# Kernel optimization log

Measured on AMD Instinct MI355X. Metric: run time of the kernel, lower is better.

Reference implementation:

```python
import jax, jax.numpy as jnp
import numpy as np

N_QUBITS = 8
EMBED_DIM = 1024
FFN_DIM = 4096


def _apply_1q_batched(state, gate, wire):
    # state: [N] + [2]*n ; gate: [N,2,2] (per-sample)
    n = state.ndim - 1
    N = state.shape[0]
    L = 2 ** wire
    R = 2 ** (n - 1 - wire)
    st = state.reshape(N, L, 2, R)
    st = jnp.einsum('nba,nlar->nlbr', gate, st)
    return st.reshape((N,) + (2,) * n)


def _apply_1q_shared(state, gate, wire):
    # gate: [2,2] shared across samples
    n = state.ndim - 1
    N = state.shape[0]
    L = 2 ** wire
    R = 2 ** (n - 1 - wire)
    st = state.reshape(N, L, 2, R)
    st = jnp.einsum('ba,nlar->nlbr', gate, st)
    return st.reshape((N,) + (2,) * n)


def _cnot(state, control, target):
    c_ax = control + 1
    t_ax = target + 1
    s0 = jnp.take(state, 0, axis=c_ax)
    s1 = jnp.take(state, 1, axis=c_ax)
    t_ax2 = t_ax - 1 if t_ax > c_ax else t_ax  # axis shift after take
    s1 = jnp.flip(s1, axis=t_ax2)
    return jnp.stack([s0, s1], axis=c_ax)


def _simulate(q_inputs, qparams):
    # q_inputs: [N, n_qubits] RX angles; qparams: [n_qubits, 3] Rot(phi,theta,omega)
    N = q_inputs.shape[0]
    n = N_QUBITS
    state = jnp.zeros((N, 2 ** n), dtype=jnp.complex64).at[:, 0].set(1.0)
    state = state.reshape((N,) + (2,) * n)
    # RX layer (per-sample angles)
    half = q_inputs.astype(jnp.float32) * 0.5
    c = jnp.cos(half).astype(jnp.complex64)
    s = (-1j) * jnp.sin(half).astype(jnp.complex64)
    for i in range(n):
        gate = jnp.stack([jnp.stack([c[:, i], s[:, i]], -1),
                          jnp.stack([s[:, i], c[:, i]], -1)], -2)  # [N,2,2]
        state = _apply_1q_batched(state, gate, i)
    # Rot layer: Rot(phi, theta, omega) = RZ(omega) RY(theta) RZ(phi)
    for i in range(n):
        phi, theta, omega = qparams[i, 0], qparams[i, 1], qparams[i, 2]
        ct = jnp.cos(theta / 2).astype(jnp.complex64)
        st = jnp.sin(theta / 2).astype(jnp.complex64)
        ep = jnp.exp(-0.5j * (phi + omega).astype(jnp.complex64))
        em = jnp.exp(0.5j * (phi - omega).astype(jnp.complex64))
        gate = jnp.array(0., jnp.complex64) + jnp.stack([
            jnp.stack([ep * ct, -em * st]),
            jnp.stack([jnp.conj(em) * st, jnp.conj(ep) * ct])])
        state = _apply_1q_shared(state, gate, i)
    # CNOT ring
    for i in range(n - 1):
        state = _cnot(state, i, i + 1)
    state = _cnot(state, n - 1, 0)
    # PauliZ expectations
    probs = jnp.abs(state) ** 2  # [N] + [2]*n, float32
    zs = []
    for i in range(n):
        axes = tuple(a for a in range(1, n + 1) if a != i + 1)
        m = probs.sum(axes)  # [N,2]
        zs.append(m[:, 0] - m[:, 1])
    return jnp.stack(zs, -1)  # [N, n_qubits]


def setup_inputs() -> dict:
    key = jax.random.key(0)
    k = jax.random.split(key, 6)
    x = jax.random.normal(k[0], (4, 2048, EMBED_DIM), dtype=jnp.float32)
    W1 = jax.random.normal(k[1], (FFN_DIM, EMBED_DIM), dtype=jnp.float32) * 0.02
    b1 = jnp.zeros((FFN_DIM,), dtype=jnp.float32)
    qparams = jax.random.normal(k[2], (N_QUBITS, 3), dtype=jnp.float32)
    W2 = jax.random.normal(k[3], (EMBED_DIM, N_QUBITS), dtype=jnp.float32) * 0.02
    b2 = jnp.zeros((EMBED_DIM,), dtype=jnp.float32)
    return {"x": x, "W1": W1, "b1": b1, "qparams": qparams, "W2": W2, "b2": b2}


def reference(x, W1, b1, qparams, W2, b2):
    batch, seq_len, embed_dim = x.shape
    x_flat = x.reshape(-1, embed_dim)
    x_ffn = x_flat @ W1.T + b1                       # [N, ffn_dim]
    q_inputs = x_ffn[:, :N_QUBITS]                   # ffn_dim >= n_qubits
    q_out = _simulate(q_inputs, qparams)             # [N, n_qubits]
    out = q_out @ W2.T + b2                          # [N, embed_dim]
    return out.reshape(batch, seq_len, embed_dim)
```

## Files before the change

### kernel.cpp

```cpp
#include <hip/hip_runtime.h>
#include <math.h>


constexpr int EMBED = 1024;
constexpr int NQ    = 8;
constexpr int ROWS  = 8;
constexpr int BLOCK = 256;

__global__ __launch_bounds__(BLOCK, 4)
void ffq_fused(const float* __restrict__ x,
               const float* __restrict__ W1,
               const float* __restrict__ b1,
               const float* __restrict__ qp,
               const float* __restrict__ W2,
               const float* __restrict__ b2,
               float* __restrict__ out,
               int total_rows)
{
    const int t    = threadIdx.x;
    const int lane = t & 63;
    const int wv   = t >> 6;
    const int c4   = t << 2;

    __shared__ float wsum[4][NQ];
    __shared__ float qoutS[NQ];

    float4 w1r[NQ];
#pragma unroll
    for (int j = 0; j < NQ; ++j)
        w1r[j] = *reinterpret_cast<const float4*>(W1 + j * EMBED + c4);

    float4 w2lo[4], w2hi[4];
#pragma unroll
    for (int i = 0; i < 4; ++i) {
        w2lo[i] = *reinterpret_cast<const float4*>(W2 + (c4 + i) * NQ);
        w2hi[i] = *reinterpret_cast<const float4*>(W2 + (c4 + i) * NQ + 4);
    }
    const float4 b2r = *reinterpret_cast<const float4*>(b2 + c4);

    float cth[NQ], ssps[NQ], b1r[NQ];
#pragma unroll
    for (int j = 0; j < NQ; ++j) {
        const float phi = qp[j * 3 + 0];
        const float th  = qp[j * 3 + 1];
        cth[j]  = cosf(th);
        ssps[j] = sinf(th) * sinf(phi);
        b1r[j]  = b1[j];
    }

    const long base = (long)blockIdx.x * ROWS;
    float4 xv = make_float4(0.f, 0.f, 0.f, 0.f);
    if (base < total_rows)
        xv = *reinterpret_cast<const float4*>(x + base * EMBED + c4);

    for (int r = 0; r < ROWS; ++r) {
        const long row = base + r;
        if (row >= total_rows) break;

        float4 xn = make_float4(0.f, 0.f, 0.f, 0.f);
        if (r + 1 < ROWS && row + 1 < total_rows)
            xn = *reinterpret_cast<const float4*>(x + (row + 1) * EMBED + c4);

        float p[NQ];
#pragma unroll
        for (int j = 0; j < NQ; ++j)
            p[j] = xv.x * w1r[j].x + xv.y * w1r[j].y +
                   xv.z * w1r[j].z + xv.w * w1r[j].w;

#pragma unroll
        for (int off = 32; off > 0; off >>= 1) {
#pragma unroll
            for (int j = 0; j < NQ; ++j)
                p[j] += __shfl_down(p[j], off, 64);
        }
        if (lane == 0) {
#pragma unroll
            for (int j = 0; j < NQ; ++j) wsum[wv][j] = p[j];
        }
        __syncthreads();

        if (t == 0) {
            float zp[NQ];
#pragma unroll
            for (int j = 0; j < NQ; ++j) {
                const float qin = wsum[0][j] + wsum[1][j] + wsum[2][j] +
                                  wsum[3][j] + b1r[j];
                float sq, cq;
                sincosf(qin, &sq, &cq);
                zp[j] = cth[j] * cq - ssps[j] * sq;
            }
            float pr = zp[0];
#pragma unroll
            for (int j = 1; j < NQ; ++j) { pr *= zp[j]; qoutS[j] = pr; }
            pr = zp[1];
#pragma unroll
            for (int j = 2; j < NQ; ++j) pr *= zp[j];
            qoutS[0] = pr;
        }
        __syncthreads();

        const float q0 = qoutS[0], q1 = qoutS[1], q2 = qoutS[2], q3 = qoutS[3];
        const float q4 = qoutS[4], q5 = qoutS[5], q6 = qoutS[6], q7 = qoutS[7];

        float4 o;
        o.x = b2r.x + q0 * w2lo[0].x + q1 * w2lo[0].y + q2 * w2lo[0].z + q3 * w2lo[0].w
                    + q4 * w2hi[0].x + q5 * w2hi[0].y + q6 * w2hi[0].z + q7 * w2hi[0].w;
        o.y = b2r.y + q0 * w2lo[1].x + q1 * w2lo[1].y + q2 * w2lo[1].z + q3 * w2lo[1].w
                    + q4 * w2hi[1].x + q5 * w2hi[1].y + q6 * w2hi[1].z + q7 * w2hi[1].w;
        o.z = b2r.z + q0 * w2lo[2].x + q1 * w2lo[2].y + q2 * w2lo[2].z + q3 * w2lo[2].w
                    + q4 * w2hi[2].x + q5 * w2hi[2].y + q6 * w2hi[2].z + q7 * w2hi[2].w;
        o.w = b2r.w + q0 * w2lo[3].x + q1 * w2lo[3].y + q2 * w2lo[3].z + q3 * w2lo[3].w
                    + q4 * w2hi[3].x + q5 * w2hi[3].y + q6 * w2hi[3].z + q7 * w2hi[3].w;

        *reinterpret_cast<float4*>(out + (size_t)row * EMBED + c4) = o;

        xv = xn;
    }
}

extern "C" void kernel_launch(void* const* d_in, const int* in_sizes, int n_in,
                              void* d_out, int out_size, void* d_ws, size_t ws_size,
                              hipStream_t stream) {
    const float* x  = (const float*)d_in[0];
    const float* W1 = (const float*)d_in[1];
    const float* b1 = (const float*)d_in[2];
    const float* qp = (const float*)d_in[3];
    const float* W2 = (const float*)d_in[4];
    const float* b2 = (const float*)d_in[5];
    float* out = (float*)d_out;

    const int rows = in_sizes[0] / EMBED;
    const int grid = (rows + ROWS - 1) / ROWS;

    hipLaunchKernelGGL(ffq_fused, dim3(grid), dim3(BLOCK), 0, stream,
                       x, W1, b1, qp, W2, b2, out, rows);
}
```

Before: 124.4 us.

## Map one wavefront per row, stage W1 in LDS, use shuffle-only reductions

Each wavefront now handles a whole row, RPW=4 rows per wave and 16 rows per block. The per-row __syncthreads and the single-thread quantum evaluation are replaced by a transpose-style shuffle reduction across lanes. The eight quantum expectation terms are computed in parallel across lanes using a folded R*cos(arg + offset) form with the hardware cosine builtin. W1 is staged in 32 KB of LDS and W2 is held in many registers. The launch bound drops to 2 blocks per SM, which may reduce occupancy, and the hardware cosine may lose some accuracy.

```diff
diff --git a/kernel.cpp b/kernel.cpp
--- a/kernel.cpp
+++ b/kernel.cpp
@@ -4,117 +4,183 @@
 
 constexpr int EMBED = 1024;
 constexpr int NQ    = 8;
-constexpr int ROWS  = 8;
 constexpr int BLOCK = 256;
-
-__global__ __launch_bounds__(BLOCK, 4)
-void ffq_fused(const float* __restrict__ x,
-               const float* __restrict__ W1,
-               const float* __restrict__ b1,
-               const float* __restrict__ qp,
-               const float* __restrict__ W2,
-               const float* __restrict__ b2,
-               float* __restrict__ out,
-               int total_rows)
+constexpr int WAVES = BLOCK / 64;
+constexpr int RPW   = 4;
+constexpr float INV2PI = 0.15915494309189535f;
+
+__global__ __launch_bounds__(BLOCK, 2)
+void ffq(const float* __restrict__ x,
+         const float* __restrict__ W1,
+         const float* __restrict__ b1,
+         const float* __restrict__ qp,
+         const float* __restrict__ W2,
+         const float* __restrict__ b2,
+         float* __restrict__ out,
+         int total_rows)
 {
     const int t    = threadIdx.x;
     const int lane = t & 63;
     const int wv   = t >> 6;
-    const int c4   = t << 2;
-
-    __shared__ float wsum[4][NQ];
-    __shared__ float qoutS[NQ];
-
-    float4 w1r[NQ];
-#pragma unroll
-    for (int j = 0; j < NQ; ++j)
-        w1r[j] = *reinterpret_cast<const float4*>(W1 + j * EMBED + c4);
-
-    float4 w2lo[4], w2hi[4];
-#pragma unroll
-    for (int i = 0; i < 4; ++i) {
-        w2lo[i] = *reinterpret_cast<const float4*>(W2 + (c4 + i) * NQ);
-        w2hi[i] = *reinterpret_cast<const float4*>(W2 + (c4 + i) * NQ + 4);
-    }
-    const float4 b2r = *reinterpret_cast<const float4*>(b2 + c4);
-
-    float cth[NQ], ssps[NQ], b1r[NQ];
-#pragma unroll
-    for (int j = 0; j < NQ; ++j) {
+
+    __shared__ float lds_w1[NQ * EMBED];
+
+    {
+        const float4* src = reinterpret_cast<const float4*>(W1);
+        float4* dst = reinterpret_cast<float4*>(lds_w1);
+#pragma unroll
+        for (int k = 0; k < (NQ * EMBED / 4) / BLOCK; ++k)
+            dst[k * BLOCK + t] = src[k * BLOCK + t];
+    }
+
+    const int j = lane & 7;
+    float Rj, qoffj;
+    {
         const float phi = qp[j * 3 + 0];
         const float th  = qp[j * 3 + 1];
-        cth[j]  = cosf(th);
-        ssps[j] = sinf(th) * sinf(phi);
-        b1r[j]  = b1[j];
-    }
-
-    const long base = (long)blockIdx.x * ROWS;
-    float4 xv = make_float4(0.f, 0.f, 0.f, 0.f);
-    if (base < total_rows)
-        xv = *reinterpret_cast<const float4*>(x + base * EMBED + c4);
-
-    for (int r = 0; r < ROWS; ++r) {
-        const long row = base + r;
+        const float cth  = cosf(th);
+        const float ssps = sinf(th) * sinf(phi);
+        Rj    = sqrtf(cth * cth + ssps * ssps);
+        qoffj = (b1[j] + atan2f(ssps, cth)) * INV2PI;
+    }
+
+    float4 w2a[4][4], w2b[4][4];
+    float4 b2f[4];
+#pragma unroll
+    for (int i = 0; i < 4; ++i) {
+        const int c = i * 256 + lane * 4;
+#pragma unroll
+        for (int q = 0; q < 4; ++q) {
+            w2a[i][q] = *reinterpret_cast<const float4*>(W2 + (c + q) * NQ);
+            w2b[i][q] = *reinterpret_cast<const float4*>(W2 + (c + q) * NQ + 4);
+        }
+        b2f[i] = *reinterpret_cast<const float4*>(b2 + c);
+    }
+
+    __syncthreads();
+
+    const int  gw = blockIdx.x * WAVES + wv;
+    const long r0 = (long)gw * RPW;
+
+    float4 xv[4];
+    if (r0 < total_rows) {
+#pragma unroll
+        for (int i = 0; i < 4; ++i)
+            xv[i] = *reinterpret_cast<const float4*>(
+                x + (size_t)r0 * EMBED + i * 256 + lane * 4);
+    }
+
+    for (int rr = 0; rr < RPW; ++rr) {
+        const long row = r0 + rr;
         if (row >= total_rows) break;
 
-        float4 xn = make_float4(0.f, 0.f, 0.f, 0.f);
-        if (r + 1 < ROWS && row + 1 < total_rows)
-            xn = *reinterpret_cast<const float4*>(x + (row + 1) * EMBED + c4);
+        float4 xn[4];
+        const bool more = (rr + 1 < RPW) && (row + 1 < total_rows);
+        if (more) {
+#pragma unroll
+            for (int i = 0; i < 4; ++i)
+                xn[i] = *reinterpret_cast<const float4*>(
+                    x + (size_t)(row + 1) * EMBED + i * 256 + lane * 4);
+        }
 
         float p[NQ];
 #pragma unroll
-        for (int j = 0; j < NQ; ++j)
-            p[j] = xv.x * w1r[j].x + xv.y * w1r[j].y +
-                   xv.z * w1r[j].z + xv.w * w1r[j].w;
-
-#pragma unroll
-        for (int off = 32; off > 0; off >>= 1) {
-#pragma unroll
-            for (int j = 0; j < NQ; ++j)
-                p[j] += __shfl_down(p[j], off, 64);
-        }
-        if (lane == 0) {
-#pragma unroll
-            for (int j = 0; j < NQ; ++j) wsum[wv][j] = p[j];
-        }
-        __syncthreads();
-
-        if (t == 0) {
-            float zp[NQ];
-#pragma unroll
-            for (int j = 0; j < NQ; ++j) {
-                const float qin = wsum[0][j] + wsum[1][j] + wsum[2][j] +
-                                  wsum[3][j] + b1r[j];
-                float sq, cq;
-                sincosf(qin, &sq, &cq);
-                zp[j] = cth[j] * cq - ssps[j] * sq;
+        for (int jj = 0; jj < NQ; ++jj) p[jj] = 0.f;
+#pragma unroll
+        for (int i = 0; i < 4; ++i) {
+#pragma unroll
+            for (int jj = 0; jj < NQ; ++jj) {
+                const float4 w = *reinterpret_cast<const float4*>(
+                    lds_w1 + jj * EMBED + i * 256 + lane * 4);
+                p[jj] += xv[i].x * w.x + xv[i].y * w.y +
+                         xv[i].z * w.z + xv[i].w * w.w;
             }
-            float pr = zp[0];
-#pragma unroll
-            for (int j = 1; j < NQ; ++j) { pr *= zp[j]; qoutS[j] = pr; }
-            pr = zp[1];
-#pragma unroll
-            for (int j = 2; j < NQ; ++j) pr *= zp[j];
-            qoutS[0] = pr;
-        }
-        __syncthreads();
-
-        const float q0 = qoutS[0], q1 = qoutS[1], q2 = qoutS[2], q3 = qoutS[3];
-        const float q4 = qoutS[4], q5 = qoutS[5], q6 = qoutS[6], q7 = qoutS[7];
-
-        float4 o;
-        o.x = b2r.x + q0 * w2lo[0].x + q1 * w2lo[0].y + q2 * w2lo[0].z + q3 * w2lo[0].w
-                    + q4 * w2hi[0].x + q5 * w2hi[0].y + q6 * w2hi[0].z + q7 * w2hi[0].w;
-        o.y = b2r.y + q0 * w2lo[1].x + q1 * w2lo[1].y + q2 * w2lo[1].z + q3 * w2lo[1].w
-                    + q4 * w2hi[1].x + q5 * w2hi[1].y + q6 * w2hi[1].z + q7 * w2hi[1].w;
-        o.z = b2r.z + q0 * w2lo[2].x + q1 * w2lo[2].y + q2 * w2lo[2].z + q3 * w2lo[2].w
-                    + q4 * w2hi[2].x + q5 * w2hi[2].y + q6 * w2hi[2].z + q7 * w2hi[2].w;
-        o.w = b2r.w + q0 * w2lo[3].x + q1 * w2lo[3].y + q2 * w2lo[3].z + q3 * w2lo[3].w
-                    + q4 * w2hi[3].x + q5 * w2hi[3].y + q6 * w2hi[3].z + q7 * w2hi[3].w;
-
-        *reinterpret_cast<float4*>(out + (size_t)row * EMBED + c4) = o;
-
-        xv = xn;
+        }
+
+        float q4[4], q2[2], tsum;
+        {
+            const bool up = (lane & 4);
+#pragma unroll
+            for (int k = 0; k < 4; ++k) {
+                const float snd = up ? p[k]     : p[k + 4];
+                const float kp  = up ? p[k + 4] : p[k];
+                q4[k] = kp + __shfl_xor(snd, 4, 64);
+            }
+        }
+        {
+            const bool up = (lane & 2);
+#pragma unroll
+            for (int k = 0; k < 2; ++k) {
+                const float snd = up ? q4[k]     : q4[k + 2];
+                const float kp  = up ? q4[k + 2] : q4[k];
+                q2[k] = kp + __shfl_xor(snd, 2, 64);
+            }
+        }
+        {
+            const bool up = (lane & 1);
+            const float snd = up ? q2[0] : q2[1];
+            const float kp  = up ? q2[1] : q2[0];
+            tsum = kp + __shfl_xor(snd, 1, 64);
+        }
+        tsum += __shfl_xor(tsum, 8, 64);
+        tsum += __shfl_xor(tsum, 16, 64);
+        tsum += __shfl_xor(tsum, 32, 64);
+
+        const float arg = tsum * INV2PI + qoffj;
+        const float zz  = Rj * __builtin_amdgcn_cosf(arg);
+
+        float z0_, z1_, z2_, z3_, z4_, z5_, z6_, z7_;
+        {
+            const float o  = __shfl_xor(zz, 1, 64);
+            const float a0 = (lane & 1) ? o  : zz;
+            const float a1 = (lane & 1) ? zz : o;
+            const float rA = __shfl_xor(a0, 2, 64);
+            const float rB = __shfl_xor(a1, 2, 64);
+            const float c0 = (lane & 2) ? rA : a0;
+            const float c1 = (lane & 2) ? rB : a1;
+            const float c2 = (lane & 2) ? a0 : rA;
+            const float c3 = (lane & 2) ? a1 : rB;
+            const float d0 = __shfl_xor(c0, 4, 64);
+            const float d1 = __shfl_xor(c1, 4, 64);
+            const float d2 = __shfl_xor(c2, 4, 64);
+            const float d3 = __shfl_xor(c3, 4, 64);
+            z0_ = (lane & 4) ? d0 : c0;
+            z1_ = (lane & 4) ? d1 : c1;
+            z2_ = (lane & 4) ? d2 : c2;
+            z3_ = (lane & 4) ? d3 : c3;
+            z4_ = (lane & 4) ? c0 : d0;
+            z5_ = (lane & 4) ? c1 : d1;
+            z6_ = (lane & 4) ? c2 : d2;
+            z7_ = (lane & 4) ? c3 : d3;
+        }
+
+        float qo0, qo1, qo2, qo3, qo4, qo5, qo6, qo7;
+        qo1 = z0_ * z1_;
+        qo2 = qo1 * z2_;
+        qo3 = qo2 * z3_;
+        qo4 = qo3 * z4_;
+        qo5 = qo4 * z5_;
+        qo6 = qo5 * z6_;
+        qo7 = qo6 * z7_;
+        qo0 = z1_ * z2_ * z3_ * z4_ * z5_ * z6_ * z7_;
+
+        float* outp = out + (size_t)row * EMBED;
+#pragma unroll
+        for (int i = 0; i < 4; ++i) {
+            float4 o = b2f[i];
+            o.x += qo0 * w2a[i][0].x + qo1 * w2a[i][0].y + qo2 * w2a[i][0].z + qo3 * w2a[i][0].w
+                 + qo4 * w2b[i][0].x + qo5 * w2b[i][0].y + qo6 * w2b[i][0].z + qo7 * w2b[i][0].w;
+            o.y += qo0 * w2a[i][1].x + qo1 * w2a[i][1].y + qo2 * w2a[i][1].z + qo3 * w2a[i][1].w
+                 + qo4 * w2b[i][1].x + qo5 * w2b[i][1].y + qo6 * w2b[i][1].z + qo7 * w2b[i][1].w;
+            o.z += qo0 * w2a[i][2].x + qo1 * w2a[i][2].y + qo2 * w2a[i][2].z + qo3 * w2a[i][2].w
+                 + qo4 * w2b[i][2].x + qo5 * w2b[i][2].y + qo6 * w2b[i][2].z + qo7 * w2b[i][2].w;
+            o.w += qo0 * w2a[i][3].x + qo1 * w2a[i][3].y + qo2 * w2a[i][3].z + qo3 * w2a[i][3].w
+                 + qo4 * w2b[i][3].x + qo5 * w2b[i][3].y + qo6 * w2b[i][3].z + qo7 * w2b[i][3].w;
+            *reinterpret_cast<float4*>(outp + i * 256 + lane * 4) = o;
+        }
+
+#pragma unroll
+        for (int i = 0; i < 4; ++i) xv[i] = xn[i];
     }
 }
 
@@ -130,8 +196,9 @@
     float* out = (float*)d_out;
 
     const int rows = in_sizes[0] / EMBED;
-    const int grid = (rows + ROWS - 1) / ROWS;
-
-    hipLaunchKernelGGL(ffq_fused, dim3(grid), dim3(BLOCK), 0, stream,
+    const int rows_per_block = WAVES * RPW;
+    const int grid = (rows + rows_per_block - 1) / rows_per_block;
+
+    hipLaunchKernelGGL(ffq, dim3(grid), dim3(BLOCK), 0, stream,
                        x, W1, b1, qp, W2, b2, out, rows);
 }
```

Measured after the change: 108.1 us. 13.1% less time.

## Split fused kernel into quantum-output kernel and output projection kernel

Applied to the files above, without the earlier changes.

Splits the single fused kernel into two. The first computes the 8 qubit expectation values per row, with a warp-level lane mapping over (qubit, quarter, row), a phase-shifted single hardware cosine instead of sincos, and shuffle-based products in place of block syncs and a serial thread-0 section. The second streams the tiny qout workspace to write the 1024-wide output. This is meant to remove the per-row __syncthreads and single-thread serialization, at the cost of an extra launch and a workspace round-trip. The fast __builtin_amdgcn_cosf may reduce accuracy for large arguments.

```diff
diff --git a/kernel.cpp b/kernel.cpp
--- a/kernel.cpp
+++ b/kernel.cpp
@@ -4,117 +4,153 @@
 
 constexpr int EMBED = 1024;
 constexpr int NQ    = 8;
-constexpr int ROWS  = 8;
-constexpr int BLOCK = 256;
+constexpr float INV2PI = 0.15915494309189535f;
 
-__global__ __launch_bounds__(BLOCK, 4)
-void ffq_fused(const float* __restrict__ x,
-               const float* __restrict__ W1,
-               const float* __restrict__ b1,
-               const float* __restrict__ qp,
-               const float* __restrict__ W2,
-               const float* __restrict__ b2,
-               float* __restrict__ out,
-               int total_rows)
+__global__ __launch_bounds__(256, 4)
+void ffq_qout(const float* __restrict__ x,
+              const float* __restrict__ W1,
+              const float* __restrict__ b1,
+              const float* __restrict__ qp,
+              float* __restrict__ qout,
+              int total_rows)
 {
     const int t    = threadIdx.x;
     const int lane = t & 63;
     const int wv   = t >> 6;
-    const int c4   = t << 2;
+    const int j    = lane & 7;
+    const int q    = (lane >> 3) & 3;
+    const int r    = lane >> 5;
 
-    __shared__ float wsum[4][NQ];
-    __shared__ float qoutS[NQ];
+    float Rj, qoffj;
+    {
+        const float phi  = qp[j * 3 + 0];
+        const float th   = qp[j * 3 + 1];
+        const float cth  = cosf(th);
+        const float ssps = sinf(th) * sinf(phi);
+        Rj    = sqrtf(cth * cth + ssps * ssps);
+        qoffj = (b1[j] + atan2f(ssps, cth)) * INV2PI;
+    }
 
-    float4 w1r[NQ];
-#pragma unroll
-    for (int j = 0; j < NQ; ++j)
-        w1r[j] = *reinterpret_cast<const float4*>(W1 + j * EMBED + c4);
+    const long rowRaw = (long)blockIdx.x * 8 + wv * 2 + r;
+    const bool rowOK  = rowRaw < total_rows;
+    const long row    = rowOK ? rowRaw : (long)(total_rows - 1);
 
-    float4 w2lo[4], w2hi[4];
+    const float* xp = x  + (size_t)row * EMBED + q * 256;
+    const float* wp = W1 + (size_t)j   * EMBED + q * 256;
+
+    float4 s = make_float4(0.f, 0.f, 0.f, 0.f);
+#pragma unroll 16
+    for (int k = 0; k < 64; ++k) {
+        const float4 xa = *reinterpret_cast<const float4*>(xp + k * 4);
+        const float4 wa = *reinterpret_cast<const float4*>(wp + k * 4);
+        s.x = fmaf(xa.x, wa.x, s.x);
+        s.y = fmaf(xa.y, wa.y, s.y);
+        s.z = fmaf(xa.z, wa.z, s.z);
+        s.w = fmaf(xa.w, wa.w, s.w);
+    }
+    float p = (s.x + s.y) + (s.z + s.w);
+
+    p += __shfl_xor(p, 8, 64);
+    p += __shfl_xor(p, 16, 64);
+
+    const float zz = Rj * __builtin_amdgcn_cosf(p * INV2PI + qoffj);
+
+    float z0_, z1_, z2_, z3_, z4_, z5_, z6_, z7_;
+    {
+        const float o  = __shfl_xor(zz, 1, 64);
+        const float a0 = (lane & 1) ? o  : zz;
+        const float a1 = (lane & 1) ? zz : o;
+        const float rA = __shfl_xor(a0, 2, 64);
+        const float rB = __shfl_xor(a1, 2, 64);
+        const float c0 = (lane & 2) ? rA : a0;
+        const float c1 = (lane & 2) ? rB : a1;
+        const float c2 = (lane & 2) ? a0 : rA;
+        const float c3 = (lane & 2) ? a1 : rB;
+        const float d0 = __shfl_xor(c0, 4, 64);
+        const float d1 = __shfl_xor(c1, 4, 64);
+        const float d2 = __shfl_xor(c2, 4, 64);
+        const float d3 = __shfl_xor(c3, 4, 64);
+        z0_ = (lane & 4) ? d0 : c0;
+        z1_ = (lane & 4) ? d1 : c1;
+        z2_ = (lane & 4) ? d2 : c2;
+        z3_ = (lane & 4) ? d3 : c3;
+        z4_ = (lane & 4) ? c0 : d0;
+        z5_ = (lane & 4) ? c1 : d1;
+        z6_ = (lane & 4) ? c2 : d2;
+        z7_ = (lane & 4) ? c3 : d3;
+    }
+
+    const float p1 = z0_ * z1_;
+    const float p2 = p1 * z2_;
+    const float p3 = p2 * z3_;
+    const float p4 = p3 * z4_;
+    const float p5 = p4 * z5_;
+    const float p6 = p5 * z6_;
+    const float p7 = p6 * z7_;
+    const float t7 = z1_ * z2_ * z3_ * z4_ * z5_ * z6_ * z7_;
+
+    float qo = p1;
+    qo = (j == 0) ? t7 : qo;
+    qo = (j == 2) ? p2 : qo;
+    qo = (j == 3) ? p3 : qo;
+    qo = (j == 4) ? p4 : qo;
+    qo = (j == 5) ? p5 : qo;
+    qo = (j == 6) ? p6 : qo;
+    qo = (j == 7) ? p7 : qo;
+
+    if (q == 0 && rowOK)
+        qout[row * NQ + j] = qo;
+}
+
+constexpr int ROWS_B = 16;
+
+__global__ __launch_bounds__(256, 2)
+void ffq_out(const float* __restrict__ qout,
+             const float* __restrict__ W2,
+             const float* __restrict__ b2,
+             float* __restrict__ out,
+             int total_rows)
+{
+    const int t   = threadIdx.x;
+    const int col = t * 4;
+
+    float4 wA[4], wB[4];
 #pragma unroll
     for (int i = 0; i < 4; ++i) {
-        w2lo[i] = *reinterpret_cast<const float4*>(W2 + (c4 + i) * NQ);
-        w2hi[i] = *reinterpret_cast<const float4*>(W2 + (c4 + i) * NQ + 4);
+        wA[i] = *reinterpret_cast<const float4*>(W2 + (col + i) * NQ);
+        wB[i] = *reinterpret_cast<const float4*>(W2 + (col + i) * NQ + 4);
     }
-    const float4 b2r = *reinterpret_cast<const float4*>(b2 + c4);
+    const float4 bb = *reinterpret_cast<const float4*>(b2 + col);
 
-    float cth[NQ], ssps[NQ], b1r[NQ];
-#pragma unroll
-    for (int j = 0; j < NQ; ++j) {
-        const float phi = qp[j * 3 + 0];
-        const float th  = qp[j * 3 + 1];
-        cth[j]  = cosf(th);
-        ssps[j] = sinf(th) * sinf(phi);
-        b1r[j]  = b1[j];
-    }
+    const long r0 = (long)blockIdx.x * ROWS_B;
+    if (r0 >= total_rows) return;
 
-    const long base = (long)blockIdx.x * ROWS;
-    float4 xv = make_float4(0.f, 0.f, 0.f, 0.f);
-    if (base < total_rows)
-        xv = *reinterpret_cast<const float4*>(x + base * EMBED + c4);
+    float4 qA = *reinterpret_cast<const float4*>(qout + r0 * NQ);
+    float4 qB = *reinterpret_cast<const float4*>(qout + r0 * NQ + 4);
 
-    for (int r = 0; r < ROWS; ++r) {
-        const long row = base + r;
+    for (int rr = 0; rr < ROWS_B; ++rr) {
+        const long row = r0 + rr;
         if (row >= total_rows) break;
 
-        float4 xn = make_float4(0.f, 0.f, 0.f, 0.f);
-        if (r + 1 < ROWS && row + 1 < total_rows)
-            xn = *reinterpret_cast<const float4*>(x + (row + 1) * EMBED + c4);
-
-        float p[NQ];
-#pragma unroll
-        for (int j = 0; j < NQ; ++j)
-            p[j] = xv.x * w1r[j].x + xv.y * w1r[j].y +
-                   xv.z * w1r[j].z + xv.w * w1r[j].w;
-
-#pragma unroll
-        for (int off = 32; off > 0; off >>= 1) {
-#pragma unroll
-            for (int j = 0; j < NQ; ++j)
-                p[j] += __shfl_down(p[j], off, 64);
+        float4 qAn = qA, qBn = qB;
+        if (rr + 1 < ROWS_B && row + 1 < total_rows) {
+            qAn = *reinterpret_cast<const float4*>(qout + (row + 1) * NQ);
+            qBn = *reinterpret_cast<const float4*>(qout + (row + 1) * NQ + 4);
         }
-        if (lane == 0) {
-#pragma unroll
-            for (int j = 0; j < NQ; ++j) wsum[wv][j] = p[j];
-        }
-        __syncthreads();
-
-        if (t == 0) {
-            float zp[NQ];
-#pragma unroll
-            for (int j = 0; j < NQ; ++j) {
-                const float qin = wsum[0][j] + wsum[1][j] + wsum[2][j] +
-                                  wsum[3][j] + b1r[j];
-                float sq, cq;
-                sincosf(qin, &sq, &cq);
-                zp[j] = cth[j] * cq - ssps[j] * sq;
-            }
-            float pr = zp[0];
-#pragma unroll
-            for (int j = 1; j < NQ; ++j) { pr *= zp[j]; qoutS[j] = pr; }
-            pr = zp[1];
-#pragma unroll
-            for (int j = 2; j < NQ; ++j) pr *= zp[j];
-            qoutS[0] = pr;
-        }
-        __syncthreads();
-
-        const float q0 = qoutS[0], q1 = qoutS[1], q2 = qoutS[2], q3 = qoutS[3];
-        const float q4 = qoutS[4], q5 = qoutS[5], q6 = qoutS[6], q7 = qoutS[7];
 
         float4 o;
-        o.x = b2r.x + q0 * w2lo[0].x + q1 * w2lo[0].y + q2 * w2lo[0].z + q3 * w2lo[0].w
-                    + q4 * w2hi[0].x + q5 * w2hi[0].y + q6 * w2hi[0].z + q7 * w2hi[0].w;
-        o.y = b2r.y + q0 * w2lo[1].x + q1 * w2lo[1].y + q2 * w2lo[1].z + q3 * w2lo[1].w
-                    + q4 * w2hi[1].x + q5 * w2hi[1].y + q6 * w2hi[1].z + q7 * w2hi[1].w;
-        o.z = b2r.z + q0 * w2lo[2].x + q1 * w2lo[2].y + q2 * w2lo[2].z + q3 * w2lo[2].w
-                    + q4 * w2hi[2].x + q5 * w2hi[2].y + q6 * w2hi[2].z + q7 * w2hi[2].w;
-        o.w = b2r.w + q0 * w2lo[3].x + q1 * w2lo[3].y + q2 * w2lo[3].z + q3 * w2lo[3].w
-                    + q4 * w2hi[3].x + q5 * w2hi[3].y + q6 * w2hi[3].z + q7 * w2hi[3].w;
+        o.x = bb.x + qA.x*wA[0].x + qA.y*wA[0].y + qA.z*wA[0].z + qA.w*wA[0].w
+                   + qB.x*wB[0].x + qB.y*wB[0].y + qB.z*wB[0].z + qB.w*wB[0].w;
+        o.y = bb.y + qA.x*wA[1].x + qA.y*wA[1].y + qA.z*wA[1].z + qA.w*wA[1].w
+                   + qB.x*wB[1].x + qB.y*wB[1].y + qB.z*wB[1].z + qB.w*wB[1].w;
+        o.z = bb.z + qA.x*wA[2].x + qA.y*wA[2].y + qA.z*wA[2].z + qA.w*wA[2].w
+                   + qB.x*wB[2].x + qB.y*wB[2].y + qB.z*wB[2].z + qB.w*wB[2].w;
+        o.w = bb.w + qA.x*wA[3].x + qA.y*wA[3].y + qA.z*wA[3].z + qA.w*wA[3].w
+                   + qB.x*wB[3].x + qB.y*wB[3].y + qB.z*wB[3].z + qB.w*wB[3].w;
 
-        *reinterpret_cast<float4*>(out + (size_t)row * EMBED + c4) = o;
+        *reinterpret_cast<float4*>(out + (size_t)row * EMBED + col) = o;
 
-        xv = xn;
+        qA = qAn; qB = qBn;
     }
 }
 
@@ -127,11 +163,15 @@
     const float* qp = (const float*)d_in[3];
     const float* W2 = (const float*)d_in[4];
     const float* b2 = (const float*)d_in[5];
-    float* out = (float*)d_out;
+    float* out  = (float*)d_out;
+    float* qout = (float*)d_ws;
 
-    const int rows = in_sizes[0] / EMBED;
-    const int grid = (rows + ROWS - 1) / ROWS;
+    const int rows  = in_sizes[0] / EMBED;
+    const int gridA = (rows + 7) / 8;
+    const int gridB = (rows + ROWS_B - 1) / ROWS_B;
 
-    hipLaunchKernelGGL(ffq_fused, dim3(grid), dim3(BLOCK), 0, stream,
-                       x, W1, b1, qp, W2, b2, out, rows);
+    hipLaunchKernelGGL(ffq_qout, dim3(gridA), dim3(256), 0, stream,
+                       x, W1, b1, qp, qout, rows);
+    hipLaunchKernelGGL(ffq_out, dim3(gridB), dim3(256), 0, stream,
+                       qout, W2, b2, out, rows);
 }
```

Result: slower. 132.4 us (+6.4%).
